# Kernel optimization log

Measured on AMD Instinct MI355X. Metric: run time of the kernel, lower is better.

The kernel has to match this reference:

```python
import jax, jax.numpy as jnp
import numpy as np

B, D, E, H, C = 2048, 1024, 8, 4096, 1024
TOP_K = 2
LN_EPS = 1e-5


def setup_inputs() -> dict:
    key = jax.random.key(0)
    ks = jax.random.split(key, 5)
    x = jax.random.normal(ks[0], (B, D), dtype=jnp.float32)
    Wr = jax.random.normal(ks[1], (D, E), dtype=jnp.float32) * 0.02
    br = jnp.zeros((E,), dtype=jnp.float32)
    ln_g = jnp.ones((E, D), dtype=jnp.float32)
    ln_b = jnp.zeros((E, D), dtype=jnp.float32)
    W1 = jax.random.normal(ks[2], (E, D, H), dtype=jnp.float32) * 0.02
    b1 = jnp.zeros((E, H), dtype=jnp.float32)
    W2 = jax.random.normal(ks[3], (E, H, C), dtype=jnp.float32) * 0.02
    b2 = jnp.zeros((E, C), dtype=jnp.float32)
    return {"x": x, "Wr": Wr, "br": br, "ln_g": ln_g, "ln_b": ln_b,
            "W1": W1, "b1": b1, "W2": W2, "b2": b2}


def reference(x, Wr, br, ln_g, ln_b, W1, b1, W2, b2):
    # Router (eval mode: no jitter)
    router_logits = x @ Wr + br                       # [B, E]
    topk_vals, topk_idx = jax.lax.top_k(router_logits, TOP_K)
    topk_w = jax.nn.softmax(topk_vals, axis=-1)       # [B, K]
    # Scatter top-k weights into a dense [B, E] combine matrix (indices unique per row)
    w_full = jnp.zeros((x.shape[0], E), dtype=x.dtype)
    w_full = w_full.at[jnp.arange(x.shape[0])[:, None], topk_idx].set(topk_w)
    # Shared LayerNorm statistics, per-expert affine
    mu = jnp.mean(x, axis=-1, keepdims=True)
    var = jnp.mean(jnp.square(x - mu), axis=-1, keepdims=True)
    xn = (x - mu) * jax.lax.rsqrt(var + LN_EPS)       # [B, D]
    xe = xn[:, None, :] * ln_g[None] + ln_b[None]     # [B, E, D]
    # Expert MLPs (dense over experts; combine weights zero-out non-selected experts)
    h = jax.nn.gelu(jnp.einsum('bed,edh->beh', xe, W1) + b1[None], approximate=False)
    y = jnp.einsum('beh,ehc->bec', h, W2) + b2[None]  # [B, E, C]
    out = jnp.einsum('be,bec->bc', w_full, y)         # weighted combine
    return out
```

## Files before the change

kernel.cpp:

```cpp
#include <hip/hip_runtime.h>
#include <hip/hip_bf16.h>

#define B_TOK 2048
#define D_DIM 1024
#define E_NUM 8
#define H_DIM 4096
#define C_DIM 1024
#define CAP   5120
#define MAXT  40

typedef __attribute__((ext_vector_type(8))) short bf16x8;
typedef __attribute__((ext_vector_type(4))) float floatx4;

__device__ __forceinline__ unsigned short f2bf(float f) {
  union { float f; unsigned int u; } a; a.f = f;
  unsigned int u = a.u;
  return (unsigned short)((u + 0x7FFFu + ((u >> 16) & 1u)) >> 16);
}

__device__ __forceinline__ void gload_lds16(const void* g, void* l) {
  __builtin_amdgcn_global_load_lds(
      (const __attribute__((address_space(1))) void*)g,
      (__attribute__((address_space(3))) void*)l, 16, 0, 0);
}

__global__ __launch_bounds__(256) void kinit(float* out_acc, int* slot_tok, int* counts) {
  int id = blockIdx.x * 256 + threadIdx.x;
  out_acc[id] = 0.f;
  if (id < CAP) slot_tok[id] = -1;
  if (id < E_NUM) counts[id] = 0;
}

__global__ __launch_bounds__(256) void krouter(const float* __restrict__ x,
                                               const float* __restrict__ Wr,
                                               const float* __restrict__ br,
                                               int2* meta_i, float4* meta_f, int* counts) {
  int b = blockIdx.x, t = threadIdx.x;
  const float4 xv = *(const float4*)(x + (size_t)b * D_DIM + t * 4);
  float v[10];
  v[0] = xv.x + xv.y + xv.z + xv.w;
  v[1] = xv.x * xv.x + xv.y * xv.y + xv.z * xv.z + xv.w * xv.w;
#pragma unroll
  for (int e = 0; e < 8; e++) v[2 + e] = 0.f;
  const float* wr = Wr + (size_t)(t * 4) * E_NUM;
  float xs[4] = {xv.x, xv.y, xv.z, xv.w};
#pragma unroll
  for (int j = 0; j < 4; j++) {
    float4 wa = *(const float4*)(wr + j * 8);
    float4 wb = *(const float4*)(wr + j * 8 + 4);
    v[2] += xs[j] * wa.x; v[3] += xs[j] * wa.y; v[4] += xs[j] * wa.z; v[5] += xs[j] * wa.w;
    v[6] += xs[j] * wb.x; v[7] += xs[j] * wb.y; v[8] += xs[j] * wb.z; v[9] += xs[j] * wb.w;
  }
#pragma unroll
  for (int i = 0; i < 10; i++) {
    float s = v[i];
#pragma unroll
    for (int off = 32; off > 0; off >>= 1) s += __shfl_down(s, off, 64);
    v[i] = s;
  }
  __shared__ float red[4][10];
  int lane = t & 63, wid = t >> 6;
  if (lane == 0) {
#pragma unroll
    for (int i = 0; i < 10; i++) red[wid][i] = v[i];
  }
  __syncthreads();
  if (t == 0) {
    float f[10];
#pragma unroll
    for (int i = 0; i < 10; i++) f[i] = red[0][i] + red[1][i] + red[2][i] + red[3][i];
    float mu = f[0] * (1.f / 1024.f);
    float var = f[1] * (1.f / 1024.f) - mu * mu;
    float rsig = rsqrtf(var + 1e-5f);
    float lg[8];
#pragma unroll
    for (int e = 0; e < 8; e++) lg[e] = f[2 + e] + br[e];
    int i0 = 0;
#pragma unroll
    for (int e = 1; e < 8; e++) if (lg[e] > lg[i0]) i0 = e;
    int i1 = (i0 == 0) ? 1 : 0;
#pragma unroll
    for (int e = 0; e < 8; e++) if (e != i0 && lg[e] > lg[i1]) i1 = e;
    float ex = expf(lg[i1] - lg[i0]);
    float w0 = 1.f / (1.f + ex);
    float w1 = 1.f - w0;
    atomicAdd(counts + i0, 1);
    atomicAdd(counts + i1, 1);
    meta_i[b] = make_int2(i0, i1);
    meta_f[b] = make_float4(w0, w1, mu, rsig);
  }
}

__global__ void kprefix(const int* counts, int* cursor, int* tmap_e, int* tmap_r) {
  if (threadIdx.x == 0) {
    int total = 0, tt = 0;
    for (int e = 0; e < E_NUM; e++) {
      cursor[e] = total;
      int nt = (counts[e] + 127) >> 7;
      for (int i = 0; i < nt; i++) { tmap_e[tt] = e; tmap_r[tt] = total + i * 128; tt++; }
      total += nt << 7;
    }
    for (; tt < MAXT; tt++) tmap_e[tt] = -1;
  }
}

__global__ __launch_bounds__(256) void kscatter(const float* __restrict__ x,
                                                const float* __restrict__ ln_g,
                                                const float* __restrict__ ln_b,
                                                const int2* __restrict__ meta_i,
                                                const float4* __restrict__ meta_f,
                                                int* cursor, int* slot_tok, float* slot_w,
                                                unsigned short* __restrict__ xe) {
  int b = blockIdx.x, t = threadIdx.x;
  __shared__ int se[2], ss[2];
  __shared__ float smu, srs;
  if (t == 0) {
    int2 mi = meta_i[b];
    float4 mf = meta_f[b];
    int s0 = atomicAdd(cursor + mi.x, 1);
    int s1 = atomicAdd(cursor + mi.y, 1);
    slot_tok[s0] = b; slot_w[s0] = mf.x;
    slot_tok[s1] = b; slot_w[s1] = mf.y;
    se[0] = mi.x; se[1] = mi.y; ss[0] = s0; ss[1] = s1;
    smu = mf.z; srs = mf.w;
  }
  __syncthreads();
  int i = t * 4;
  float4 xv = *(const float4*)(x + (size_t)b * D_DIM + i);
  float mu = smu, rs = srs;
  float xn0 = (xv.x - mu) * rs, xn1 = (xv.y - mu) * rs, xn2 = (xv.z - mu) * rs, xn3 = (xv.w - mu) * rs;
#pragma unroll
  for (int k = 0; k < 2; k++) {
    int e = se[k], s = ss[k];
    float4 g = *(const float4*)(ln_g + (size_t)e * D_DIM + i);
    float4 bb = *(const float4*)(ln_b + (size_t)e * D_DIM + i);
    union { unsigned short us[4]; uint2 v; } u;
    u.us[0] = f2bf(xn0 * g.x + bb.x);
    u.us[1] = f2bf(xn1 * g.y + bb.y);
    u.us[2] = f2bf(xn2 * g.z + bb.z);
    u.us[3] = f2bf(xn3 * g.w + bb.w);
    *(uint2*)(xe + (size_t)s * D_DIM + i) = u.v;
  }
}

__global__ __launch_bounds__(256) void ktranspose(const float* __restrict__ src,
                                                  unsigned short* __restrict__ dst,
                                                  int R, int C) {
  __shared__ float tile[64][65];
  int z = blockIdx.z;
  const float* s = src + (size_t)z * R * C;
  unsigned short* d = dst + (size_t)z * R * C;
  int cx = blockIdx.x * 64, ry = blockIdx.y * 64;
  int t = threadIdx.x;
  int cl4 = (t & 15) * 4, rl = t >> 4;
#pragma unroll
  for (int p = 0; p < 4; p++) {
    int r = rl + p * 16;
    float4 v = *(const float4*)(s + (size_t)(ry + r) * C + cx + cl4);
    tile[r][cl4] = v.x; tile[r][cl4 + 1] = v.y; tile[r][cl4 + 2] = v.z; tile[r][cl4 + 3] = v.w;
  }
  __syncthreads();
#pragma unroll
  for (int p = 0; p < 4; p++) {
    int c = rl + p * 16;
    union { unsigned short us[4]; uint2 v; } u;
    u.us[0] = f2bf(tile[cl4][c]);
    u.us[1] = f2bf(tile[cl4 + 1][c]);
    u.us[2] = f2bf(tile[cl4 + 2][c]);
    u.us[3] = f2bf(tile[cl4 + 3][c]);
    *(uint2*)(d + (size_t)(cx + c) * R + ry + cl4) = u.v;
  }
}

__global__ __launch_bounds__(256) void kgemm1(const unsigned short* __restrict__ xe,
                                              const unsigned short* __restrict__ w1t,
                                              const float* __restrict__ b1,
                                              unsigned short* __restrict__ h,
                                              const int* __restrict__ tmap_e,
                                              const int* __restrict__ tmap_r) {
  int e = tmap_e[blockIdx.y];
  if (e < 0) return;
  int row0 = tmap_r[blockIdx.y];
  int n0 = blockIdx.x * 128;
  const unsigned short* Ab = xe + (size_t)row0 * D_DIM;
  const unsigned short* Bb = w1t + (size_t)e * H_DIM * D_DIM + (size_t)n0 * D_DIM;
  __shared__ unsigned short As[128 * 32];
  __shared__ unsigned short Bs[128 * 32];
  int t = threadIdx.x, lane = t & 63, wid = t >> 6;
  int c0 = wid * 2, c1 = c0 + 1;
  int lr0 = c0 * 16 + (lane >> 2);
  int kc = (lane & 3) * 8;
  const unsigned short* ga0 = Ab + (size_t)lr0 * D_DIM + kc;
  const unsigned short* ga1 = ga0 + 16 * D_DIM;
  const unsigned short* gb0 = Bb + (size_t)lr0 * D_DIM + kc;
  const unsigned short* gb1 = gb0 + 16 * D_DIM;
  unsigned short* la0 = As + c0 * 512;
  unsigned short* la1 = As + c1 * 512;
  unsigned short* lb0 = Bs + c0 * 512;
  unsigned short* lb1 = Bs + c1 * 512;
  int l15 = lane & 15, q = lane >> 4;
  int wm = (wid & 1) * 64, wn = (wid >> 1) * 64;
  const unsigned short* pa[4];
  const unsigned short* pb[4];
#pragma unroll
  for (int i = 0; i < 4; i++) {
    pa[i] = As + (wm + i * 16 + l15) * 32 + q * 8;
    pb[i] = Bs + (wn + i * 16 + l15) * 32 + q * 8;
  }
  floatx4 acc[4][4];
#pragma unroll
  for (int i = 0; i < 4; i++)
#pragma unroll
    for (int j = 0; j < 4; j++) acc[i][j] = (floatx4){0.f, 0.f, 0.f, 0.f};

  for (int k0 = 0; k0 < D_DIM; k0 += 32) {
    gload_lds16(ga0, la0);
    gload_lds16(ga1, la1);
    gload_lds16(gb0, lb0);
    gload_lds16(gb1, lb1);
    __syncthreads();
    bf16x8 af[4], bfr[4];
#pragma unroll
    for (int i = 0; i < 4; i++) { af[i] = *(const bf16x8*)pa[i]; bfr[i] = *(const bf16x8*)pb[i]; }
#pragma unroll
    for (int mt = 0; mt < 4; mt++)
#pragma unroll
      for (int nt = 0; nt < 4; nt++)
        acc[mt][nt] = __builtin_amdgcn_mfma_f32_16x16x32_bf16(af[mt], bfr[nt], acc[mt][nt], 0, 0, 0);
    __syncthreads();
    ga0 += 32; ga1 += 32; gb0 += 32; gb1 += 32;
  }
  float b1v[4];
#pragma unroll
  for (int nt = 0; nt < 4; nt++) b1v[nt] = b1[(size_t)e * H_DIM + n0 + wn + nt * 16 + l15];
#pragma unroll
  for (int mt = 0; mt < 4; mt++) {
    int row = row0 + wm + mt * 16 + q * 4;
#pragma unroll
    for (int nt = 0; nt < 4; nt++) {
      int col = n0 + wn + nt * 16 + l15;
      unsigned short* hp = h + (size_t)row * H_DIM + col;
#pragma unroll
      for (int r = 0; r < 4; r++) {
        float v = acc[mt][nt][r] + b1v[nt];
        v = 0.5f * v * (1.f + erff(v * 0.70710678118f));
        hp[(size_t)r * H_DIM] = f2bf(v);
      }
    }
  }
}

__global__ __launch_bounds__(256) void kgemm2(const unsigned short* __restrict__ h,
                                              const unsigned short* __restrict__ w2t,
                                              const int* __restrict__ slot_tok,
                                              const float* __restrict__ slot_w,
                                              float* __restrict__ out_acc,
                                              const int* __restrict__ tmap_e,
                                              const int* __restrict__ tmap_r) {
  int e = tmap_e[blockIdx.y];
  if (e < 0) return;
  int row0 = tmap_r[blockIdx.y];
  int n0 = blockIdx.x * 128;
  int kz = blockIdx.z;
  const unsigned short* Ab = h + (size_t)row0 * H_DIM + kz * 2048;
  const unsigned short* Bb = w2t + (size_t)e * C_DIM * H_DIM + (size_t)n0 * H_DIM + kz * 2048;
  __shared__ unsigned short As[128 * 32];
  __shared__ unsigned short Bs[128 * 32];
  __shared__ int stok[128];
  __shared__ float swgt[128];
  int t = threadIdx.x, lane = t & 63, wid = t >> 6;
  if (t < 128) { stok[t] = slot_tok[row0 + t]; swgt[t] = slot_w[row0 + t]; }
  int c0 = wid * 2, c1 = c0 + 1;
  int lr0 = c0 * 16 + (lane >> 2);
  int kc = (lane & 3) * 8;
  const unsigned short* ga0 = Ab + (size_t)lr0 * H_DIM + kc;
  const unsigned short* ga1 = ga0 + (size_t)16 * H_DIM;
  const unsigned short* gb0 = Bb + (size_t)lr0 * H_DIM + kc;
  const unsigned short* gb1 = gb0 + (size_t)16 * H_DIM;
  unsigned short* la0 = As + c0 * 512;
  unsigned short* la1 = As + c1 * 512;
  unsigned short* lb0 = Bs + c0 * 512;
  unsigned short* lb1 = Bs + c1 * 512;
  int l15 = lane & 15, q = lane >> 4;
  int wm = (wid & 1) * 64, wn = (wid >> 1) * 64;
  const unsigned short* pa[4];
  const unsigned short* pb[4];
#pragma unroll
  for (int i = 0; i < 4; i++) {
    pa[i] = As + (wm + i * 16 + l15) * 32 + q * 8;
    pb[i] = Bs + (wn + i * 16 + l15) * 32 + q * 8;
  }
  floatx4 acc[4][4];
#pragma unroll
  for (int i = 0; i < 4; i++)
#pragma unroll
    for (int j = 0; j < 4; j++) acc[i][j] = (floatx4){0.f, 0.f, 0.f, 0.f};

  for (int k0 = 0; k0 < 2048; k0 += 32) {
    gload_lds16(ga0, la0);
    gload_lds16(ga1, la1);
    gload_lds16(gb0, lb0);
    gload_lds16(gb1, lb1);
    __syncthreads();
    bf16x8 af[4], bfr[4];
#pragma unroll
    for (int i = 0; i < 4; i++) { af[i] = *(const bf16x8*)pa[i]; bfr[i] = *(const bf16x8*)pb[i]; }
#pragma unroll
    for (int mt = 0; mt < 4; mt++)
#pragma unroll
      for (int nt = 0; nt < 4; nt++)
        acc[mt][nt] = __builtin_amdgcn_mfma_f32_16x16x32_bf16(af[mt], bfr[nt], acc[mt][nt], 0, 0, 0);
    __syncthreads();
    ga0 += 32; ga1 += 32; gb0 += 32; gb1 += 32;
  }
#pragma unroll
  for (int mt = 0; mt < 4; mt++) {
    int rbase = wm + mt * 16 + q * 4;
#pragma unroll
    for (int nt = 0; nt < 4; nt++) {
      int col = n0 + wn + nt * 16 + l15;
#pragma unroll
      for (int r = 0; r < 4; r++) {
        int tk = stok[rbase + r];
        if (tk >= 0)
          atomicAdd(out_acc + (size_t)tk * C_DIM + col, swgt[rbase + r] * acc[mt][nt][r]);
      }
    }
  }
}

__global__ __launch_bounds__(256) void kfinal(const float* __restrict__ out_acc,
                                              const int2* __restrict__ meta_i,
                                              const float4* __restrict__ meta_f,
                                              const float* __restrict__ b2,
                                              float* __restrict__ out) {
  int b = blockIdx.x, t = threadIdx.x;
  int i = t * 4;
  int2 mi = meta_i[b];
  float4 mf = meta_f[b];
  float4 a = *(const float4*)(out_acc + (size_t)b * C_DIM + i);
  float4 p = *(const float4*)(b2 + (size_t)mi.x * C_DIM + i);
  float4 qv = *(const float4*)(b2 + (size_t)mi.y * C_DIM + i);
  float4 o;
  o.x = a.x + mf.x * p.x + mf.y * qv.x;
  o.y = a.y + mf.x * p.y + mf.y * qv.y;
  o.z = a.z + mf.x * p.z + mf.y * qv.z;
  o.w = a.w + mf.x * p.w + mf.y * qv.w;
  *(float4*)(out + (size_t)b * C_DIM + i) = o;
}

extern "C" void kernel_launch(void* const* d_in, const int* in_sizes, int n_in,
                              void* d_out, int out_size, void* d_ws, size_t ws_size,
                              hipStream_t stream) {
  const float* x    = (const float*)d_in[0];
  const float* Wr   = (const float*)d_in[1];
  const float* br   = (const float*)d_in[2];
  const float* ln_g = (const float*)d_in[3];
  const float* ln_b = (const float*)d_in[4];
  const float* W1   = (const float*)d_in[5];
  const float* b1   = (const float*)d_in[6];
  const float* W2   = (const float*)d_in[7];
  const float* b2   = (const float*)d_in[8];

  char* w = (char*)d_ws;
  auto alloc = [&](size_t sz) { char* p = w; w += (sz + 255) & ~(size_t)255; return p; };
  unsigned short* W1t = (unsigned short*)alloc((size_t)E_NUM * H_DIM * D_DIM * 2);
  unsigned short* W2t = (unsigned short*)alloc((size_t)E_NUM * C_DIM * H_DIM * 2);
  unsigned short* xe  = (unsigned short*)alloc((size_t)CAP * D_DIM * 2);
  unsigned short* hb  = (unsigned short*)alloc((size_t)CAP * H_DIM * 2);
  float* out_acc      = (float*)alloc((size_t)B_TOK * C_DIM * 4);
  int2* meta_i        = (int2*)alloc((size_t)B_TOK * 8);
  float4* meta_f      = (float4*)alloc((size_t)B_TOK * 16);
  int* counts         = (int*)alloc(64);
  int* cursor         = (int*)alloc(64);
  int* tmap_e         = (int*)alloc(MAXT * 4);
  int* tmap_r         = (int*)alloc(MAXT * 4);
  int* slot_tok       = (int*)alloc(CAP * 4);
  float* slot_w       = (float*)alloc(CAP * 4);

  hipLaunchKernelGGL(ktranspose, dim3(H_DIM / 64, D_DIM / 64, E_NUM), dim3(256), 0, stream,
                     W1, W1t, D_DIM, H_DIM);
  hipLaunchKernelGGL(ktranspose, dim3(C_DIM / 64, H_DIM / 64, E_NUM), dim3(256), 0, stream,
                     W2, W2t, H_DIM, C_DIM);
  hipLaunchKernelGGL(kinit, dim3(B_TOK * C_DIM / 256), dim3(256), 0, stream,
                     out_acc, slot_tok, counts);
  hipLaunchKernelGGL(krouter, dim3(B_TOK), dim3(256), 0, stream,
                     x, Wr, br, meta_i, meta_f, counts);
  hipLaunchKernelGGL(kprefix, dim3(1), dim3(64), 0, stream,
                     counts, cursor, tmap_e, tmap_r);
  hipLaunchKernelGGL(kscatter, dim3(B_TOK), dim3(256), 0, stream,
                     x, ln_g, ln_b, meta_i, meta_f, cursor, slot_tok, slot_w, xe);
  hipLaunchKernelGGL(kgemm1, dim3(H_DIM / 128, MAXT), dim3(256), 0, stream,
                     xe, W1t, b1, hb, tmap_e, tmap_r);
  hipLaunchKernelGGL(kgemm2, dim3(C_DIM / 128, MAXT, 2), dim3(256), 0, stream,
                     hb, W2t, slot_tok, slot_w, out_acc, tmap_e, tmap_r);
  hipLaunchKernelGGL(kfinal, dim3(B_TOK), dim3(256), 0, stream,
                     out_acc, meta_i, meta_f, b2, (float*)d_out);
}
```

Before: 577.8 us.

## Replace atomic scatter-combine with split-K partial buffers and swizzle GEMM LDS layouts

```diff
diff --git a/kernel.cpp b/kernel.cpp
--- a/kernel.cpp
+++ b/kernel.cpp
@@ -8,6 +8,7 @@
 #define C_DIM 1024
 #define CAP   5120
 #define MAXT  40
+#define KZ    4
 
 typedef __attribute__((ext_vector_type(8))) short bf16x8;
 typedef __attribute__((ext_vector_type(4))) float floatx4;
@@ -18,17 +19,19 @@
   return (unsigned short)((u + 0x7FFFu + ((u >> 16) & 1u)) >> 16);
 }
 
+__device__ __forceinline__ float fast_erf(float x) {
+  float ax = fabsf(x);
+  float t = 1.f / fmaf(0.3275911f, ax, 1.f);
+  float y = t * fmaf(t, fmaf(t, fmaf(t, fmaf(t, 1.061405429f, -1.453152027f),
+                                     1.421413741f), -0.284496736f), 0.254829592f);
+  float r = 1.f - y * __expf(-ax * ax);
+  return copysignf(r, x);
+}
+
 __device__ __forceinline__ void gload_lds16(const void* g, void* l) {
   __builtin_amdgcn_global_load_lds(
       (const __attribute__((address_space(1))) void*)g,
       (__attribute__((address_space(3))) void*)l, 16, 0, 0);
-}
-
-__global__ __launch_bounds__(256) void kinit(float* out_acc, int* slot_tok, int* counts) {
-  int id = blockIdx.x * 256 + threadIdx.x;
-  out_acc[id] = 0.f;
-  if (id < CAP) slot_tok[id] = -1;
-  if (id < E_NUM) counts[id] = 0;
 }
 
 __global__ __launch_bounds__(256) void krouter(const float* __restrict__ x,
@@ -109,7 +112,7 @@
                                                 const float* __restrict__ ln_b,
                                                 const int2* __restrict__ meta_i,
                                                 const float4* __restrict__ meta_f,
-                                                int* cursor, int* slot_tok, float* slot_w,
+                                                int* cursor, int2* meta_s,
                                                 unsigned short* __restrict__ xe) {
   int b = blockIdx.x, t = threadIdx.x;
   __shared__ int se[2], ss[2];
@@ -119,8 +122,7 @@
     float4 mf = meta_f[b];
     int s0 = atomicAdd(cursor + mi.x, 1);
     int s1 = atomicAdd(cursor + mi.y, 1);
-    slot_tok[s0] = b; slot_w[s0] = mf.x;
-    slot_tok[s1] = b; slot_w[s1] = mf.y;
+    meta_s[b] = make_int2(s0, s1);
     se[0] = mi.x; se[1] = mi.y; ss[0] = s0; ss[1] = s1;
     smu = mf.z; srs = mf.w;
   }
@@ -145,13 +147,15 @@
 
 __global__ __launch_bounds__(256) void ktranspose(const float* __restrict__ src,
                                                   unsigned short* __restrict__ dst,
-                                                  int R, int C) {
+                                                  int R, int C, int* counts) {
   __shared__ float tile[64][65];
+  int t = threadIdx.x;
+  if (counts && blockIdx.x == 0 && blockIdx.y == 0 && blockIdx.z == 0 && t < E_NUM)
+    counts[t] = 0;
   int z = blockIdx.z;
   const float* s = src + (size_t)z * R * C;
   unsigned short* d = dst + (size_t)z * R * C;
   int cx = blockIdx.x * 64, ry = blockIdx.y * 64;
-  int t = threadIdx.x;
   int cl4 = (t & 15) * 4, rl = t >> 4;
 #pragma unroll
   for (int p = 0; p < 4; p++) {
@@ -160,15 +164,14 @@
     tile[r][cl4] = v.x; tile[r][cl4 + 1] = v.y; tile[r][cl4 + 2] = v.z; tile[r][cl4 + 3] = v.w;
   }
   __syncthreads();
-#pragma unroll
-  for (int p = 0; p < 4; p++) {
-    int c = rl + p * 16;
-    union { unsigned short us[4]; uint2 v; } u;
-    u.us[0] = f2bf(tile[cl4][c]);
-    u.us[1] = f2bf(tile[cl4 + 1][c]);
-    u.us[2] = f2bf(tile[cl4 + 2][c]);
-    u.us[3] = f2bf(tile[cl4 + 3][c]);
-    *(uint2*)(d + (size_t)(cx + c) * R + ry + cl4) = u.v;
+  int cg = t >> 3, r0 = (t & 7) * 8;
+#pragma unroll
+  for (int round = 0; round < 2; round++) {
+    int c = cg + round * 32;
+    union { unsigned short us[8]; uint4 v; } u;
+#pragma unroll
+    for (int j = 0; j < 8; j++) u.us[j] = f2bf(tile[r0 + j][c]);
+    *(uint4*)(d + (size_t)(cx + c) * R + ry + r0) = u.v;
   }
 }
 
@@ -178,21 +181,24 @@
                                               unsigned short* __restrict__ h,
                                               const int* __restrict__ tmap_e,
                                               const int* __restrict__ tmap_r) {
-  int e = tmap_e[blockIdx.y];
+  int orig = blockIdx.y * 32 + blockIdx.x;
+  int s = (orig & 7) * 160 + (orig >> 3);
+  int bx = s & 31, by = s >> 5;
+  int e = tmap_e[by];
   if (e < 0) return;
-  int row0 = tmap_r[blockIdx.y];
-  int n0 = blockIdx.x * 128;
+  int row0 = tmap_r[by];
+  int n0 = bx * 128;
   const unsigned short* Ab = xe + (size_t)row0 * D_DIM;
   const unsigned short* Bb = w1t + (size_t)e * H_DIM * D_DIM + (size_t)n0 * D_DIM;
   __shared__ unsigned short As[128 * 32];
   __shared__ unsigned short Bs[128 * 32];
   int t = threadIdx.x, lane = t & 63, wid = t >> 6;
   int c0 = wid * 2, c1 = c0 + 1;
-  int lr0 = c0 * 16 + (lane >> 2);
-  int kc = (lane & 3) * 8;
-  const unsigned short* ga0 = Ab + (size_t)lr0 * D_DIM + kc;
+  int lr = lane >> 2;
+  int kc = ((lane & 3) ^ ((lane >> 3) & 3)) * 8;
+  const unsigned short* ga0 = Ab + (size_t)(c0 * 16 + lr) * D_DIM + kc;
   const unsigned short* ga1 = ga0 + 16 * D_DIM;
-  const unsigned short* gb0 = Bb + (size_t)lr0 * D_DIM + kc;
+  const unsigned short* gb0 = Bb + (size_t)(c0 * 16 + lr) * D_DIM + kc;
   const unsigned short* gb1 = gb0 + 16 * D_DIM;
   unsigned short* la0 = As + c0 * 512;
   unsigned short* la1 = As + c1 * 512;
@@ -200,12 +206,13 @@
   unsigned short* lb1 = Bs + c1 * 512;
   int l15 = lane & 15, q = lane >> 4;
   int wm = (wid & 1) * 64, wn = (wid >> 1) * 64;
-  const unsigned short* pa[4];
-  const unsigned short* pb[4];
+  int offA[4], offB[4];
 #pragma unroll
   for (int i = 0; i < 4; i++) {
-    pa[i] = As + (wm + i * 16 + l15) * 32 + q * 8;
-    pb[i] = Bs + (wn + i * 16 + l15) * 32 + q * 8;
+    int ra = wm + i * 16 + l15;
+    int rb = wn + i * 16 + l15;
+    offA[i] = ra * 32 + ((q ^ ((ra >> 1) & 3)) * 8);
+    offB[i] = rb * 32 + ((q ^ ((rb >> 1) & 3)) * 8);
   }
   floatx4 acc[4][4];
 #pragma unroll
@@ -221,7 +228,7 @@
     __syncthreads();
     bf16x8 af[4], bfr[4];
 #pragma unroll
-    for (int i = 0; i < 4; i++) { af[i] = *(const bf16x8*)pa[i]; bfr[i] = *(const bf16x8*)pb[i]; }
+    for (int i = 0; i < 4; i++) { af[i] = *(const bf16x8*)(&As[offA[i]]); bfr[i] = *(const bf16x8*)(&Bs[offB[i]]); }
 #pragma unroll
     for (int mt = 0; mt < 4; mt++)
 #pragma unroll
@@ -243,7 +250,7 @@
 #pragma unroll
       for (int r = 0; r < 4; r++) {
         float v = acc[mt][nt][r] + b1v[nt];
-        v = 0.5f * v * (1.f + erff(v * 0.70710678118f));
+        v = 0.5f * v * (1.f + fast_erf(v * 0.70710678118f));
         hp[(size_t)r * H_DIM] = f2bf(v);
       }
     }
@@ -252,30 +259,30 @@
 
 __global__ __launch_bounds__(256) void kgemm2(const unsigned short* __restrict__ h,
                                               const unsigned short* __restrict__ w2t,
-                                              const int* __restrict__ slot_tok,
-                                              const float* __restrict__ slot_w,
-                                              float* __restrict__ out_acc,
+                                              float* __restrict__ y_parts,
                                               const int* __restrict__ tmap_e,
                                               const int* __restrict__ tmap_r) {
-  int e = tmap_e[blockIdx.y];
+  int orig = (blockIdx.z * MAXT + blockIdx.y) * 8 + blockIdx.x;
+  int s = (orig & 7) * 160 + (orig >> 3);
+  int bx = s & 7;
+  int rest = s >> 3;
+  int by = rest % MAXT;
+  int kz = rest / MAXT;
+  int e = tmap_e[by];
   if (e < 0) return;
-  int row0 = tmap_r[blockIdx.y];
-  int n0 = blockIdx.x * 128;
-  int kz = blockIdx.z;
-  const unsigned short* Ab = h + (size_t)row0 * H_DIM + kz * 2048;
-  const unsigned short* Bb = w2t + (size_t)e * C_DIM * H_DIM + (size_t)n0 * H_DIM + kz * 2048;
+  int row0 = tmap_r[by];
+  int n0 = bx * 128;
+  const unsigned short* Ab = h + (size_t)row0 * H_DIM + kz * 1024;
+  const unsigned short* Bb = w2t + (size_t)e * C_DIM * H_DIM + (size_t)n0 * H_DIM + kz * 1024;
   __shared__ unsigned short As[128 * 32];
   __shared__ unsigned short Bs[128 * 32];
-  __shared__ int stok[128];
-  __shared__ float swgt[128];
   int t = threadIdx.x, lane = t & 63, wid = t >> 6;
-  if (t < 128) { stok[t] = slot_tok[row0 + t]; swgt[t] = slot_w[row0 + t]; }
   int c0 = wid * 2, c1 = c0 + 1;
-  int lr0 = c0 * 16 + (lane >> 2);
-  int kc = (lane & 3) * 8;
-  const unsigned short* ga0 = Ab + (size_t)lr0 * H_DIM + kc;
+  int lr = lane >> 2;
+  int kc = ((lane & 3) ^ ((lane >> 3) & 3)) * 8;
+  const unsigned short* ga0 = Ab + (size_t)(c0 * 16 + lr) * H_DIM + kc;
   const unsigned short* ga1 = ga0 + (size_t)16 * H_DIM;
-  const unsigned short* gb0 = Bb + (size_t)lr0 * H_DIM + kc;
+  const unsigned short* gb0 = Bb + (size_t)(c0 * 16 + lr) * H_DIM + kc;
   const unsigned short* gb1 = gb0 + (size_t)16 * H_DIM;
   unsigned short* la0 = As + c0 * 512;
   unsigned short* la1 = As + c1 * 512;
@@ -283,12 +290,13 @@
   unsigned short* lb1 = Bs + c1 * 512;
   int l15 = lane & 15, q = lane >> 4;
   int wm = (wid & 1) * 64, wn = (wid >> 1) * 64;
-  const unsigned short* pa[4];
-  const unsigned short* pb[4];
+  int offA[4], offB[4];
 #pragma unroll
   for (int i = 0; i < 4; i++) {
-    pa[i] = As + (wm + i * 16 + l15) * 32 + q * 8;
-    pb[i] = Bs + (wn + i * 16 + l15) * 32 + q * 8;
+    int ra = wm + i * 16 + l15;
+    int rb = wn + i * 16 + l15;
+    offA[i] = ra * 32 + ((q ^ ((ra >> 1) & 3)) * 8);
+    offB[i] = rb * 32 + ((q ^ ((rb >> 1) & 3)) * 8);
   }
   floatx4 acc[4][4];
 #pragma unroll
@@ -296,7 +304,7 @@
 #pragma unroll
     for (int j = 0; j < 4; j++) acc[i][j] = (floatx4){0.f, 0.f, 0.f, 0.f};
 
-  for (int k0 = 0; k0 < 2048; k0 += 32) {
+  for (int k0 = 0; k0 < 1024; k0 += 32) {
     gload_lds16(ga0, la0);
     gload_lds16(ga1, la1);
     gload_lds16(gb0, lb0);
@@ -304,7 +312,7 @@
     __syncthreads();
     bf16x8 af[4], bfr[4];
 #pragma unroll
-    for (int i = 0; i < 4; i++) { af[i] = *(const bf16x8*)pa[i]; bfr[i] = *(const bf16x8*)pb[i]; }
+    for (int i = 0; i < 4; i++) { af[i] = *(const bf16x8*)(&As[offA[i]]); bfr[i] = *(const bf16x8*)(&Bs[offB[i]]); }
 #pragma unroll
     for (int mt = 0; mt < 4; mt++)
 #pragma unroll
@@ -313,6 +321,7 @@
     __syncthreads();
     ga0 += 32; ga1 += 32; gb0 += 32; gb1 += 32;
   }
+  float* yp = y_parts + ((size_t)kz * CAP + row0) * C_DIM;
 #pragma unroll
   for (int mt = 0; mt < 4; mt++) {
     int rbase = wm + mt * 16 + q * 4;
@@ -320,32 +329,39 @@
     for (int nt = 0; nt < 4; nt++) {
       int col = n0 + wn + nt * 16 + l15;
 #pragma unroll
-      for (int r = 0; r < 4; r++) {
-        int tk = stok[rbase + r];
-        if (tk >= 0)
-          atomicAdd(out_acc + (size_t)tk * C_DIM + col, swgt[rbase + r] * acc[mt][nt][r]);
-      }
+      for (int r = 0; r < 4; r++)
+        yp[(size_t)(rbase + r) * C_DIM + col] = acc[mt][nt][r];
     }
   }
 }
 
-__global__ __launch_bounds__(256) void kfinal(const float* __restrict__ out_acc,
+__global__ __launch_bounds__(256) void kfinal(const float* __restrict__ y_parts,
                                               const int2* __restrict__ meta_i,
+                                              const int2* __restrict__ meta_s,
                                               const float4* __restrict__ meta_f,
                                               const float* __restrict__ b2,
                                               float* __restrict__ out) {
   int b = blockIdx.x, t = threadIdx.x;
   int i = t * 4;
   int2 mi = meta_i[b];
+  int2 ms = meta_s[b];
   float4 mf = meta_f[b];
-  float4 a = *(const float4*)(out_acc + (size_t)b * C_DIM + i);
+  float a0x = 0.f, a0y = 0.f, a0z = 0.f, a0w = 0.f;
+  float a1x = 0.f, a1y = 0.f, a1z = 0.f, a1w = 0.f;
+#pragma unroll
+  for (int kz = 0; kz < KZ; kz++) {
+    float4 p = *(const float4*)(y_parts + ((size_t)kz * CAP + ms.x) * C_DIM + i);
+    float4 qv = *(const float4*)(y_parts + ((size_t)kz * CAP + ms.y) * C_DIM + i);
+    a0x += p.x; a0y += p.y; a0z += p.z; a0w += p.w;
+    a1x += qv.x; a1y += qv.y; a1z += qv.z; a1w += qv.w;
+  }
   float4 p = *(const float4*)(b2 + (size_t)mi.x * C_DIM + i);
   float4 qv = *(const float4*)(b2 + (size_t)mi.y * C_DIM + i);
   float4 o;
-  o.x = a.x + mf.x * p.x + mf.y * qv.x;
-  o.y = a.y + mf.x * p.y + mf.y * qv.y;
-  o.z = a.z + mf.x * p.z + mf.y * qv.z;
-  o.w = a.w + mf.x * p.w + mf.y * qv.w;
+  o.x = mf.x * (a0x + p.x) + mf.y * (a1x + qv.x);
+  o.y = mf.x * (a0y + p.y) + mf.y * (a1y + qv.y);
+  o.z = mf.x * (a0z + p.z) + mf.y * (a1z + qv.z);
+  o.w = mf.x * (a0w + p.w) + mf.y * (a1w + qv.w);
   *(float4*)(out + (size_t)b * C_DIM + i) = o;
 }
 
@@ -364,36 +380,36 @@
 
   char* w = (char*)d_ws;
   auto alloc = [&](size_t sz) { char* p = w; w += (sz + 255) & ~(size_t)255; return p; };
-  unsigned short* W1t = (unsigned short*)alloc((size_t)E_NUM * H_DIM * D_DIM * 2);
+  size_t sz_w1t = (size_t)E_NUM * H_DIM * D_DIM * 2;
+  size_t sz_yp  = (size_t)KZ * CAP * C_DIM * 4;
+  char* shared_region = alloc(sz_yp > sz_w1t ? sz_yp : sz_w1t);
+  unsigned short* W1t = (unsigned short*)shared_region;
+  float* y_parts      = (float*)shared_region;
   unsigned short* W2t = (unsigned short*)alloc((size_t)E_NUM * C_DIM * H_DIM * 2);
   unsigned short* xe  = (unsigned short*)alloc((size_t)CAP * D_DIM * 2);
   unsigned short* hb  = (unsigned short*)alloc((size_t)CAP * H_DIM * 2);
-  float* out_acc      = (float*)alloc((size_t)B_TOK * C_DIM * 4);
   int2* meta_i        = (int2*)alloc((size_t)B_TOK * 8);
   float4* meta_f      = (float4*)alloc((size_t)B_TOK * 16);
+  int2* meta_s        = (int2*)alloc((size_t)B_TOK * 8);
   int* counts         = (int*)alloc(64);
   int* cursor         = (int*)alloc(64);
   int* tmap_e         = (int*)alloc(MAXT * 4);
   int* tmap_r         = (int*)alloc(MAXT * 4);
-  int* slot_tok       = (int*)alloc(CAP * 4);
-  float* slot_w       = (float*)alloc(CAP * 4);
 
   hipLaunchKernelGGL(ktranspose, dim3(H_DIM / 64, D_DIM / 64, E_NUM), dim3(256), 0, stream,
-                     W1, W1t, D_DIM, H_DIM);
+                     W1, W1t, D_DIM, H_DIM, counts);
   hipLaunchKernelGGL(ktranspose, dim3(C_DIM / 64, H_DIM / 64, E_NUM), dim3(256), 0, stream,
-                     W2, W2t, H_DIM, C_DIM);
-  hipLaunchKernelGGL(kinit, dim3(B_TOK * C_DIM / 256), dim3(256), 0, stream,
-                     out_acc, slot_tok, counts);
+                     W2, W2t, H_DIM, C_DIM, (int*)nullptr);
   hipLaunchKernelGGL(krouter, dim3(B_TOK), dim3(256), 0, stream,
                      x, Wr, br, meta_i, meta_f, counts);
   hipLaunchKernelGGL(kprefix, dim3(1), dim3(64), 0, stream,
                      counts, cursor, tmap_e, tmap_r);
   hipLaunchKernelGGL(kscatter, dim3(B_TOK), dim3(256), 0, stream,
-                     x, ln_g, ln_b, meta_i, meta_f, cursor, slot_tok, slot_w, xe);
+                     x, ln_g, ln_b, meta_i, meta_f, cursor, meta_s, xe);
   hipLaunchKernelGGL(kgemm1, dim3(H_DIM / 128, MAXT), dim3(256), 0, stream,
                      xe, W1t, b1, hb, tmap_e, tmap_r);
-  hipLaunchKernelGGL(kgemm2, dim3(C_DIM / 128, MAXT, 2), dim3(256), 0, stream,
-                     hb, W2t, slot_tok, slot_w, out_acc, tmap_e, tmap_r);
+  hipLaunchKernelGGL(kgemm2, dim3(C_DIM / 128, MAXT, KZ), dim3(256), 0, stream,
+                     hb, W2t, y_parts, tmap_e, tmap_r);
   hipLaunchKernelGGL(kfinal, dim3(B_TOK), dim3(256), 0, stream,
-                     out_acc, meta_i, meta_f, b2, (float*)d_out);
-}
+                     y_parts, meta_i, meta_s, meta_f, b2, (float*)d_out);
+}
```

Result: slower. 592.6 us (+2.6%).
